# Kernel optimization log

Hardware: AMD Instinct MI355X
Metric: run time of the kernel (lower is better)

## Reference

```python
import jax, jax.numpy as jnp
import numpy as np

# Static config matching AdaConv(c_in=512, p=4, batch_size=8, s_d=512, c_out=512)
C_IN = 512
C_OUT = 512
N_GROUPS = 128  # c_in // p


def _conv(x, w, b, groups=1, padding='VALID'):
    # x: NCHW, w: OIHW
    y = jax.lax.conv_general_dilated(
        x, w, window_strides=(1, 1), padding=padding,
        dimension_numbers=('NCHW', 'OIHW', 'NCHW'),
        feature_group_count=groups)
    return y + b[None, :, None, None]


def setup_inputs() -> dict:
    key = jax.random.key(0)
    ks = jax.random.split(key, 9)
    f32 = jnp.float32
    s = 0.02  # small init scale to keep activations well-behaved
    inp = {
        'style_encoding': jax.random.normal(ks[0], (8, 512, 4, 4), f32),
        'predicted': jax.random.normal(ks[1], (8, 512, 64, 64), f32),
        'dw1_w': jax.random.normal(ks[2], (512, 512, 1, 1), f32) * s,
        'dw1_b': jnp.full((512,), 0.01, f32),
        'dw2_w': jax.random.normal(ks[3], (2048, 512, 2, 2), f32) * s,
        'dw2_b': jnp.full((2048,), 0.01, f32),
        'pk1_w': jax.random.normal(ks[4], (512, 512, 1, 1), f32) * s,
        'pk1_b': jnp.full((512,), 0.01, f32),
        'pk2_w': jax.random.normal(ks[5], (2048, 512, 1, 1), f32) * s,
        'pk2_b': jnp.full((2048,), 0.01, f32),
        'pb1_w': jax.random.normal(ks[6], (512, 512, 1, 1), f32) * s,
        'pb1_b': jnp.full((512,), 0.01, f32),
        'pb2_w': jax.random.normal(ks[7], (512, 512, 1, 1), f32) * s,
        'pb2_b': jnp.full((512,), 0.01, f32),
    }
    return inp


def reference(style_encoding, predicted,
              dw1_w, dw1_b, dw2_w, dw2_b,
              pk1_w, pk1_b, pk2_w, pk2_b,
              pb1_w, pb1_b, pb2_w, pb2_b):
    N = style_encoding.shape[0]
    lrelu = lambda x: jax.nn.leaky_relu(x, 0.01)

    # --- predict per-sample depthwise 3x3 kernels from style (4x4 -> 3x3) ---
    h = lrelu(_conv(style_encoding, dw1_w, dw1_b))           # [N, c_in, 4, 4]
    depthwise = _conv(h, dw2_w, dw2_b)                       # [N, c_out*(c_in/n_groups), 3, 3]
    depthwise = depthwise.reshape(N * C_OUT, C_IN // N_GROUPS, 3, 3)

    # --- predict per-sample pointwise kernels + bias from pooled style ---
    s_pool = jnp.mean(style_encoding, axis=(2, 3), keepdims=True)  # [N, s_d, 1, 1]
    pk = _conv(lrelu(_conv(s_pool, pk1_w, pk1_b)), pk2_w, pk2_b)
    pointwise_kn = pk.reshape(N * C_OUT, C_OUT // N_GROUPS, 1, 1)
    pb = _conv(lrelu(_conv(s_pool, pb1_w, pb1_b)), pb2_w, pb2_b)
    pointwise_bias = pb.reshape(N * C_OUT)

    # --- apply per-sample dynamic conv via huge-group grouped conv trick ---
    a, b, c, d = predicted.shape
    x = predicted.reshape(1, a * b, c, d)
    x = jnp.pad(x, ((0, 0), (0, 0), (1, 1), (1, 1)), mode='reflect')
    batch_groups = N * N_GROUPS
    y = jax.lax.conv_general_dilated(
        x, depthwise, (1, 1), 'VALID',
        dimension_numbers=('NCHW', 'OIHW', 'NCHW'),
        feature_group_count=batch_groups)                    # [1, N*c_out, c, d]
    y = jax.lax.conv_general_dilated(
        y, pointwise_kn, (1, 1), 'VALID',
        dimension_numbers=('NCHW', 'OIHW', 'NCHW'),
        feature_group_count=batch_groups)
    y = y + pointwise_bias[None, :, None, None]
    # permute([1,0,2,3]).view(a,b,c,d) with leading dim 1 == plain reshape
    return y.reshape(a, b, c, d)
```

## Files before the change

### kernel.cpp

```cpp
#include <hip/hip_runtime.h>

#define LRELU(x) ((x) > 0.f ? (x) : 0.01f * (x))

#define H2_OFF    0
#define T1_OFF    65536
#define T2_OFF    69632
#define PK_OFF    73728
#define PB_OFF    90112
#define WB_OFF    241664

__global__ __launch_bounds__(256) void kA(const float* __restrict__ style,
    const float* __restrict__ dw1_w, const float* __restrict__ dw1_b,
    const float* __restrict__ pk1_w, const float* __restrict__ pk1_b,
    const float* __restrict__ pb1_w, const float* __restrict__ pb1_b,
    float* __restrict__ h2t, float* __restrict__ t1, float* __restrict__ t2) {
  int b = blockIdx.x;
  int tid = threadIdx.x;
  __shared__ float smem[512];
  int wave = tid >> 6, l = tid & 63;
  float sv[8];
  if (b < 512) {
    int n = b >> 6; int pix = (b >> 2) & 15; int cq = b & 3;
    const float* sp = style + n * 8192 + pix;
#pragma unroll
    for (int j = 0; j < 8; ++j) sv[j] = sp[(8 * l + j) * 16];
    int cobase = cq * 128 + wave * 32;
    float res = (l < 32) ? dw1_b[cobase + l] : 0.f;
#pragma unroll 8
    for (int j = 0; j < 32; ++j) {
      const float4* wr = (const float4*)(dw1_w + (cobase + j) * 512 + 8 * l);
      float4 a = wr[0], c = wr[1];
      float v = a.x*sv[0] + a.y*sv[1] + a.z*sv[2] + a.w*sv[3]
              + c.x*sv[4] + c.y*sv[5] + c.z*sv[6] + c.w*sv[7];
      v += __shfl_xor(v, 1);
      v += __shfl_xor(v, 2);
      v += __shfl_xor(v, 4);
      v += __shfl_xor(v, 8);
      v += __shfl_xor(v, 16);
      v += __shfl_xor(v, 32);
      if (l == j) res += v;
    }
    if (l < 32) h2t[n * 8192 + (cobase + l) * 16 + pix] = LRELU(res);
  } else {
    int b2 = b - 512;
    int cq = b2 & 3; int which = (b2 >> 2) & 1; int n = b2 >> 3;
    for (int ci = tid; ci < 512; ci += 256) {
      const float4* r4 = (const float4*)(style + n * 8192 + ci * 16);
      float4 a = r4[0], bb = r4[1], c = r4[2], d = r4[3];
      smem[ci] = (a.x+a.y+a.z+a.w + bb.x+bb.y+bb.z+bb.w + c.x+c.y+c.z+c.w + d.x+d.y+d.z+d.w) * (1.f/16.f);
    }
    __syncthreads();
#pragma unroll
    for (int j = 0; j < 8; ++j) sv[j] = smem[8 * l + j];
    const float* w  = which ? pb1_w : pk1_w;
    const float* bv = which ? pb1_b : pk1_b;
    int cobase = cq * 128 + wave * 32;
    float* outp = (which ? t2 : t1) + n * 512;
    float res = (l < 32) ? bv[cobase + l] : 0.f;
#pragma unroll 8
    for (int j = 0; j < 32; ++j) {
      const float4* wr = (const float4*)(w + (cobase + j) * 512 + 8 * l);
      float4 a = wr[0], c = wr[1];
      float v = a.x*sv[0] + a.y*sv[1] + a.z*sv[2] + a.w*sv[3]
              + c.x*sv[4] + c.y*sv[5] + c.z*sv[6] + c.w*sv[7];
      v += __shfl_xor(v, 1);
      v += __shfl_xor(v, 2);
      v += __shfl_xor(v, 4);
      v += __shfl_xor(v, 8);
      v += __shfl_xor(v, 16);
      v += __shfl_xor(v, 32);
      if (l == j) res += v;
    }
    if (l < 32) outp[cobase + l] = LRELU(res);
  }
}

__global__ __launch_bounds__(256) void kB(const float* __restrict__ h2t,
    const float* __restrict__ dw2_w,
    const float* __restrict__ t1, const float* __restrict__ t2,
    const float* __restrict__ pk2_w, const float* __restrict__ pk2_b,
    const float* __restrict__ pb2_w, const float* __restrict__ pb2_b,
    float* __restrict__ PART, float* __restrict__ pk, float* __restrict__ pb) {
  __shared__ float smem[2592];
  int b = blockIdx.x;
  int tid = threadIdx.x;
  if (b < 512) {
    int bo = b & 15; int kc = b >> 4;
    float* ht = smem;
    {
      int f4 = tid * 2;
#pragma unroll
      for (int j = 0; j < 2; ++j) {
        int fi = f4 + j;
        int n = fi >> 6; int rem = fi & 63; int ci = rem >> 2; int q = rem & 3;
        float4 v = *(const float4*)(h2t + (size_t)n * 8192 + (kc * 16 + ci) * 16 + q * 4);
        *(float4*)&ht[n * 324 + ci * 20 + q * 4] = v;
      }
    }
    __syncthreads();
    int og = tid & 31; int n = tid >> 5;
    const float* hb = &ht[n * 324];
    int o2b = bo * 128 + og * 4;
    const float* wbase = dw2_w + (size_t)o2b * 2048 + kc * 64;
    float acc[9][4];
#pragma unroll
    for (int p = 0; p < 9; ++p)
#pragma unroll
      for (int oj = 0; oj < 4; ++oj) acc[p][oj] = 0.f;
#pragma unroll 2
    for (int ci = 0; ci < 16; ++ci) {
      const float* hr = hb + ci * 20;
      float4 a0 = *(const float4*)(hr);
      float4 a1 = *(const float4*)(hr + 4);
      float4 a2 = *(const float4*)(hr + 8);
      float4 a3 = *(const float4*)(hr + 12);
#pragma unroll
      for (int oj = 0; oj < 4; ++oj) {
        float4 w = *(const float4*)(wbase + (size_t)oj * 2048 + ci * 4);
        acc[0][oj] += w.x*a0.x + w.y*a0.y + w.z*a1.x + w.w*a1.y;
        acc[1][oj] += w.x*a0.y + w.y*a0.z + w.z*a1.y + w.w*a1.z;
        acc[2][oj] += w.x*a0.z + w.y*a0.w + w.z*a1.z + w.w*a1.w;
        acc[3][oj] += w.x*a1.x + w.y*a1.y + w.z*a2.x + w.w*a2.y;
        acc[4][oj] += w.x*a1.y + w.y*a1.z + w.z*a2.y + w.w*a2.z;
        acc[5][oj] += w.x*a1.z + w.y*a1.w + w.z*a2.z + w.w*a2.w;
        acc[6][oj] += w.x*a2.x + w.y*a2.y + w.z*a3.x + w.w*a3.y;
        acc[7][oj] += w.x*a2.y + w.y*a2.z + w.z*a3.y + w.w*a3.z;
        acc[8][oj] += w.x*a2.z + w.y*a2.w + w.z*a3.z + w.w*a3.w;
      }
    }
#pragma unroll
    for (int p = 0; p < 9; ++p) {
      float4 st; st.x = acc[p][0]; st.y = acc[p][1]; st.z = acc[p][2]; st.w = acc[p][3];
      *(float4*)&PART[(size_t)kc * 147456 + (size_t)(n * 9 + p) * 2048 + o2b] = st;
    }
  } else {
    int b2 = b - 512;
    int n = b2 / 20; int t20 = b2 % 20;
    bool isPb = t20 >= 16;
    int cobase = (isPb ? (t20 - 16) : t20) * 128;
    float* s = smem;
    const float* src = (isPb ? t2 : t1) + n * 512;
    for (int i = tid; i < 512; i += 256) s[i] = src[i];
    __syncthreads();
    int wave = tid >> 6, l = tid & 63;
    float sv[8];
#pragma unroll
    for (int j = 0; j < 8; ++j) sv[j] = s[8 * l + j];
    const float* w  = isPb ? pb2_w : pk2_w;
    const float* bv = isPb ? pb2_b : pk2_b;
    int cg = cobase + wave * 32;
    float res = (l < 32) ? bv[cg + l] : 0.f;
#pragma unroll 8
    for (int j = 0; j < 32; ++j) {
      const float4* wr = (const float4*)(w + (cg + j) * 512 + 8 * l);
      float4 a = wr[0], c = wr[1];
      float v = a.x*sv[0] + a.y*sv[1] + a.z*sv[2] + a.w*sv[3]
              + c.x*sv[4] + c.y*sv[5] + c.z*sv[6] + c.w*sv[7];
      v += __shfl_xor(v, 1);
      v += __shfl_xor(v, 2);
      v += __shfl_xor(v, 4);
      v += __shfl_xor(v, 8);
      v += __shfl_xor(v, 16);
      v += __shfl_xor(v, 32);
      if (l == j) res += v;
    }
    if (l < 32) {
      if (isPb) pb[n * 512 + cg + l] = res;
      else      pk[n * 2048 + cg + l] = res;
    }
  }
}

__global__ __launch_bounds__(256) void kW(const float* __restrict__ PART,
    const float* __restrict__ pk, const float* __restrict__ dw2_b,
    const float* __restrict__ pb, float* __restrict__ wbuf) {
  int idx = blockIdx.x * 256 + threadIdx.x;
  if (idx >= 8 * 128 * 160) return;
  int t = idx % 160; int Qn = idx / 160; int Q = Qn & 127; int n = Qn >> 7;
  if (t >= 144) {
    wbuf[idx] = (t < 148) ? pb[n * 512 + Q * 4 + (t - 144)] : 0.f;
    return;
  }
  int o = t & 3; int u = t >> 2; int kx = u % 3; int v = u / 3;
  int i = v & 3; int ky = v >> 2; int p = ky * 3 + kx;
  const float* pkp = pk + n * 2048 + 16 * Q + 4 * o;
  const float* bp  = dw2_b + 16 * Q;
  size_t dbase = (size_t)(n * 9 + p) * 2048 + 16 * Q;
  float sum = 0.f;
#pragma unroll
  for (int j = 0; j < 4; ++j) {
    float dv = bp[4 * j + i];
    size_t off = dbase + 4 * j + i;
#pragma unroll
    for (int s = 0; s < 32; ++s) dv += PART[(size_t)s * 147456 + off];
    sum += pkp[j] * dv;
  }
  wbuf[idx] = sum;
}

__global__ __launch_bounds__(256) void kC(const float* __restrict__ x,
    const float* __restrict__ wbuf, float* __restrict__ out) {
  int b = blockIdx.x; int rt = b & 3; int Q = (b >> 2) & 127; int n = b >> 9;
  const float* wb = wbuf + (size_t)(n * 128 + Q) * 160;
  const float* base = x + (size_t)(n * 512 + Q * 4) * 4096;
  int e = threadIdx.x & 15;
  int y = rt * 16 + (threadIdx.x >> 4);
  int x0 = 4 * e;
  int ro[3];
#pragma unroll
  for (int ky = 0; ky < 3; ++ky) {
    int ry = y - 1 + ky;
    ry = ry < 0 ? 1 : (ry > 63 ? 62 : ry);
    ro[ky] = ry * 64;
  }
  float4 v[4][3];
#pragma unroll
  for (int i = 0; i < 4; ++i)
#pragma unroll
    for (int ky = 0; ky < 3; ++ky)
      v[i][ky] = *(const float4*)(base + i * 4096 + ro[ky] + x0);
  float acc[4][4];
#pragma unroll
  for (int o = 0; o < 4; ++o) {
    float bv = wb[144 + o];
#pragma unroll
    for (int px = 0; px < 4; ++px) acc[o][px] = bv;
  }
#pragma unroll
  for (int i = 0; i < 4; ++i) {
#pragma unroll
    for (int ky = 0; ky < 3; ++ky) {
      float vl = __shfl_up(v[i][ky].w, 1, 16);
      float vr = __shfl_down(v[i][ky].x, 1, 16);
      if (e == 0)  vl = v[i][ky].y;
      if (e == 15) vr = v[i][ky].z;
      float va0 = vl, va1 = v[i][ky].x, va2 = v[i][ky].y, va3 = v[i][ky].z,
            va4 = v[i][ky].w, va5 = vr;
#pragma unroll
      for (int kx = 0; kx < 3; ++kx) {
        const float* wp = &wb[((ky * 4 + i) * 3 + kx) * 4];
        float w0 = wp[0], w1 = wp[1], w2 = wp[2], w3 = wp[3];
        float xv0 = kx == 0 ? va0 : (kx == 1 ? va1 : va2);
        float xv1 = kx == 0 ? va1 : (kx == 1 ? va2 : va3);
        float xv2 = kx == 0 ? va2 : (kx == 1 ? va3 : va4);
        float xv3 = kx == 0 ? va3 : (kx == 1 ? va4 : va5);
        acc[0][0] += w0 * xv0; acc[0][1] += w0 * xv1; acc[0][2] += w0 * xv2; acc[0][3] += w0 * xv3;
        acc[1][0] += w1 * xv0; acc[1][1] += w1 * xv1; acc[1][2] += w1 * xv2; acc[1][3] += w1 * xv3;
        acc[2][0] += w2 * xv0; acc[2][1] += w2 * xv1; acc[2][2] += w2 * xv2; acc[2][3] += w2 * xv3;
        acc[3][0] += w3 * xv0; acc[3][1] += w3 * xv1; acc[3][2] += w3 * xv2; acc[3][3] += w3 * xv3;
      }
    }
  }
#pragma unroll
  for (int o = 0; o < 4; ++o) {
    float4 st; st.x = acc[o][0]; st.y = acc[o][1]; st.z = acc[o][2]; st.w = acc[o][3];
    *(float4*)&out[(((size_t)(n * 512 + Q * 4 + o)) * 64 + y) * 64 + x0] = st;
  }
}

extern "C" void kernel_launch(void* const* d_in, const int* in_sizes, int n_in,
                              void* d_out, int out_size, void* d_ws, size_t ws_size,
                              hipStream_t stream) {
  const float* style = (const float*)d_in[0];
  const float* pred  = (const float*)d_in[1];
  const float* dw1_w = (const float*)d_in[2];
  const float* dw1_b = (const float*)d_in[3];
  const float* dw2_w = (const float*)d_in[4];
  const float* dw2_b = (const float*)d_in[5];
  const float* pk1_w = (const float*)d_in[6];
  const float* pk1_b = (const float*)d_in[7];
  const float* pk2_w = (const float*)d_in[8];
  const float* pk2_b = (const float*)d_in[9];
  const float* pb1_w = (const float*)d_in[10];
  const float* pb1_b = (const float*)d_in[11];
  const float* pb2_w = (const float*)d_in[12];
  const float* pb2_b = (const float*)d_in[13];
  float* ws  = (float*)d_ws;
  float* h2t = ws + H2_OFF;
  float* t1  = ws + T1_OFF;
  float* t2  = ws + T2_OFF;
  float* pk  = ws + PK_OFF;
  float* pb  = ws + PB_OFF;
  float* wb  = ws + WB_OFF;
  float* out = (float*)d_out;
  float* PART = out;

  kA<<<576, 256, 0, stream>>>(style, dw1_w, dw1_b, pk1_w, pk1_b, pb1_w, pb1_b, h2t, t1, t2);
  kB<<<672, 256, 0, stream>>>(h2t, dw2_w, t1, t2, pk2_w, pk2_b, pb2_w, pb2_b, PART, pk, pb);
  kW<<<640, 256, 0, stream>>>(PART, pk, dw2_b, pb, wb);
  kC<<<4096, 256, 0, stream>>>(pred, wb, out);
}
```

Before: 74.42 us.

## Stage depthwise input tiles in LDS with double-buffered async loads

```diff
diff --git a/kernel.cpp b/kernel.cpp
--- a/kernel.cpp
+++ b/kernel.cpp
@@ -200,62 +200,95 @@
 
 __global__ __launch_bounds__(256) void kC(const float* __restrict__ x,
     const float* __restrict__ wbuf, float* __restrict__ out) {
-  int b = blockIdx.x; int rt = b & 3; int Q = (b >> 2) & 127; int n = b >> 9;
+  int b = blockIdx.x; int Q = b & 127; int n = b >> 7;
   const float* wb = wbuf + (size_t)(n * 128 + Q) * 160;
   const float* base = x + (size_t)(n * 512 + Q * 4) * 4096;
-  int e = threadIdx.x & 15;
-  int y = rt * 16 + (threadIdx.x >> 4);
+  __shared__ float xs[2][4608];
+  int tid = threadIdx.x;
+  int e = tid & 15;
+  int r = (tid >> 4) & 15;
+  int wave = tid >> 6, l = tid & 63;
   int x0 = 4 * e;
-  int ro[3];
-#pragma unroll
-  for (int ky = 0; ky < 3; ++ky) {
-    int ry = y - 1 + ky;
-    ry = ry < 0 ? 1 : (ry > 63 ? 62 : ry);
-    ro[ky] = ry * 64;
-  }
-  float4 v[4][3];
-#pragma unroll
-  for (int i = 0; i < 4; ++i)
-#pragma unroll
-    for (int ky = 0; ky < 3; ++ky)
-      v[i][ky] = *(const float4*)(base + i * 4096 + ro[ky] + x0);
-  float acc[4][4];
-#pragma unroll
-  for (int o = 0; o < 4; ++o) {
-    float bv = wb[144 + o];
-#pragma unroll
-    for (int px = 0; px < 4; ++px) acc[o][px] = bv;
-  }
-#pragma unroll
-  for (int i = 0; i < 4; ++i) {
-#pragma unroll
-    for (int ky = 0; ky < 3; ++ky) {
-      float vl = __shfl_up(v[i][ky].w, 1, 16);
-      float vr = __shfl_down(v[i][ky].x, 1, 16);
-      if (e == 0)  vl = v[i][ky].y;
-      if (e == 15) vr = v[i][ky].z;
-      float va0 = vl, va1 = v[i][ky].x, va2 = v[i][ky].y, va3 = v[i][ky].z,
-            va4 = v[i][ky].w, va5 = vr;
-#pragma unroll
-      for (int kx = 0; kx < 3; ++kx) {
-        const float* wp = &wb[((ky * 4 + i) * 3 + kx) * 4];
-        float w0 = wp[0], w1 = wp[1], w2 = wp[2], w3 = wp[3];
-        float xv0 = kx == 0 ? va0 : (kx == 1 ? va1 : va2);
-        float xv1 = kx == 0 ? va1 : (kx == 1 ? va2 : va3);
-        float xv2 = kx == 0 ? va2 : (kx == 1 ? va3 : va4);
-        float xv3 = kx == 0 ? va3 : (kx == 1 ? va4 : va5);
-        acc[0][0] += w0 * xv0; acc[0][1] += w0 * xv1; acc[0][2] += w0 * xv2; acc[0][3] += w0 * xv3;
-        acc[1][0] += w1 * xv0; acc[1][1] += w1 * xv1; acc[1][2] += w1 * xv2; acc[1][3] += w1 * xv3;
-        acc[2][0] += w2 * xv0; acc[2][1] += w2 * xv1; acc[2][2] += w2 * xv2; acc[2][3] += w2 * xv3;
-        acc[3][0] += w3 * xv0; acc[3][1] += w3 * xv1; acc[3][2] += w3 * xv2; acc[3][3] += w3 * xv3;
-      }
-    }
-  }
-#pragma unroll
-  for (int o = 0; o < 4; ++o) {
-    float4 st; st.x = acc[o][0]; st.y = acc[o][1]; st.z = acc[o][2]; st.w = acc[o][3];
-    *(float4*)&out[(((size_t)(n * 512 + Q * 4 + o)) * 64 + y) * 64 + x0] = st;
-  }
+
+#define STAGE(BUF, T)                                                          \
+  for (int c = wave; c < 18; c += 4) {                                         \
+    int q = c * 256 + l * 4;                                                   \
+    int ch = q / 1152;                                                         \
+    int rem = q - ch * 1152;                                                   \
+    int rr = rem >> 6;                                                         \
+    int gx = rem & 63;                                                         \
+    int gy = (T) * 16 + rr - 1;                                                \
+    gy = gy < 0 ? 1 : (gy > 63 ? 62 : gy);                                     \
+    const float* srcp = base + ch * 4096 + gy * 64 + gx;                       \
+    __builtin_amdgcn_global_load_lds(                                          \
+        (const __attribute__((address_space(1))) unsigned int*)srcp,           \
+        (__attribute__((address_space(3))) unsigned int*)&xs[BUF][c * 256],    \
+        16, 0, 0);                                                             \
+  }
+
+#define COMPUTE(BUF, T)                                                        \
+  {                                                                            \
+    int y = (T) * 16 + r;                                                      \
+    float acc[4][4];                                                           \
+    _Pragma("unroll")                                                          \
+    for (int o = 0; o < 4; ++o) {                                              \
+      float bv = wb[144 + o];                                                  \
+      _Pragma("unroll")                                                        \
+      for (int px = 0; px < 4; ++px) acc[o][px] = bv;                          \
+    }                                                                          \
+    _Pragma("unroll")                                                          \
+    for (int i = 0; i < 4; ++i) {                                              \
+      _Pragma("unroll")                                                        \
+      for (int ky = 0; ky < 3; ++ky) {                                         \
+        float4 vv = *(const float4*)&xs[BUF][i * 1152 + (r + ky) * 64 + x0];   \
+        float vl = __shfl_up(vv.w, 1, 16);                                     \
+        float vr = __shfl_down(vv.x, 1, 16);                                   \
+        if (e == 0)  vl = vv.y;                                                \
+        if (e == 15) vr = vv.z;                                                \
+        float va0 = vl, va1 = vv.x, va2 = vv.y, va3 = vv.z, va4 = vv.w,        \
+              va5 = vr;                                                        \
+        _Pragma("unroll")                                                      \
+        for (int kx = 0; kx < 3; ++kx) {                                       \
+          const float* wp = &wb[((ky * 4 + i) * 3 + kx) * 4];                  \
+          float w0 = wp[0], w1 = wp[1], w2 = wp[2], w3 = wp[3];                \
+          float xv0 = kx == 0 ? va0 : (kx == 1 ? va1 : va2);                   \
+          float xv1 = kx == 0 ? va1 : (kx == 1 ? va2 : va3);                   \
+          float xv2 = kx == 0 ? va2 : (kx == 1 ? va3 : va4);                   \
+          float xv3 = kx == 0 ? va3 : (kx == 1 ? va4 : va5);                   \
+          acc[0][0] += w0 * xv0; acc[0][1] += w0 * xv1;                        \
+          acc[0][2] += w0 * xv2; acc[0][3] += w0 * xv3;                        \
+          acc[1][0] += w1 * xv0; acc[1][1] += w1 * xv1;                        \
+          acc[1][2] += w1 * xv2; acc[1][3] += w1 * xv3;                        \
+          acc[2][0] += w2 * xv0; acc[2][1] += w2 * xv1;                        \
+          acc[2][2] += w2 * xv2; acc[2][3] += w2 * xv3;                        \
+          acc[3][0] += w3 * xv0; acc[3][1] += w3 * xv1;                        \
+          acc[3][2] += w3 * xv2; acc[3][3] += w3 * xv3;                        \
+        }                                                                      \
+      }                                                                        \
+    }                                                                          \
+    _Pragma("unroll")                                                          \
+    for (int o = 0; o < 4; ++o) {                                              \
+      float4 st; st.x = acc[o][0]; st.y = acc[o][1];                           \
+      st.z = acc[o][2]; st.w = acc[o][3];                                      \
+      *(float4*)&out[(((size_t)(n * 512 + Q * 4 + o)) * 64 + y) * 64 + x0]     \
+          = st;                                                                \
+    }                                                                          \
+  }
+
+  STAGE(0, 0)
+  __syncthreads();
+  STAGE(1, 1)
+  COMPUTE(0, 0)
+  __syncthreads();
+  STAGE(0, 2)
+  COMPUTE(1, 1)
+  __syncthreads();
+  STAGE(1, 3)
+  COMPUTE(0, 2)
+  __syncthreads();
+  COMPUTE(1, 3)
+#undef STAGE
+#undef COMPUTE
 }
 
 extern "C" void kernel_launch(void* const* d_in, const int* in_sizes, int n_in,
@@ -288,5 +321,5 @@
   kA<<<576, 256, 0, stream>>>(style, dw1_w, dw1_b, pk1_w, pk1_b, pb1_w, pb1_b, h2t, t1, t2);
   kB<<<672, 256, 0, stream>>>(h2t, dw2_w, t1, t2, pk2_w, pk2_b, pb2_w, pb2_b, PART, pk, pb);
   kW<<<640, 256, 0, stream>>>(PART, pk, dw2_b, pb, wb);
-  kC<<<4096, 256, 0, stream>>>(pred, wb, out);
-}
+  kC<<<1024, 256, 0, stream>>>(pred, wb, out);
+}
```

After: 78.10 us. 1.05x slower.
